# Performance work log

Measured on AMD Instinct MI355X. Metric: run time of the kernel, lower is better.

## Reference

```python
import jax, jax.numpy as jnp
import numpy as np

DIM = 1024
N_HEADS = 16
N_KV = 4
HEAD_DIM = 64
HIDDEN = 2048
N_EXP = 8
TOP_K = 2
B, T = 2, 1024
EPS = 1e-6


def rmsnorm(x, w):
    rms = jnp.sqrt(jnp.mean(x * x, axis=-1, keepdims=True) + EPS)
    return w * x / rms


def apply_rope(x, cos, sin):
    # x: [B, H, T, D]; cos/sin: [T, D//2]
    Tn = x.shape[2]
    c = cos[None, None, :Tn, :]
    s = sin[None, None, :Tn, :]
    xe = x[..., 0::2]
    xo = x[..., 1::2]
    re = xe * c - xo * s
    ro = xe * s + xo * c
    return jnp.stack([re, ro], axis=-1).reshape(x.shape)


def setup_inputs() -> dict:
    key = jax.random.key(0)
    ks = jax.random.split(key, 12)
    sd = DIM ** -0.5
    x = jax.random.normal(ks[0], (B, T, DIM), dtype=jnp.float32)
    # RoPE tables
    half = HEAD_DIM // 2
    inv_freq = 1.0 / (10000.0 ** (np.arange(0, half, dtype=np.float32) / half))
    pos = np.arange(T, dtype=np.float32)
    ang = np.outer(pos, inv_freq)
    cos = jnp.asarray(np.cos(ang), dtype=jnp.float32)
    sin = jnp.asarray(np.sin(ang), dtype=jnp.float32)
    return {
        "x": x,
        "cos": cos,
        "sin": sin,
        "norm_attn_w": jnp.ones((DIM,), jnp.float32),
        "wq": jax.random.normal(ks[1], (N_HEADS * HEAD_DIM, DIM), jnp.float32) * sd,
        "wk": jax.random.normal(ks[2], (N_KV * HEAD_DIM, DIM), jnp.float32) * sd,
        "wv": jax.random.normal(ks[3], (N_KV * HEAD_DIM, DIM), jnp.float32) * sd,
        "wo": jax.random.normal(ks[4], (DIM, N_HEADS * HEAD_DIM), jnp.float32) * sd,
        "norm_ffn_w": jnp.ones((DIM,), jnp.float32),
        "router_w": jax.random.normal(ks[5], (N_EXP, DIM), jnp.float32) * sd,
        "router_b": jnp.zeros((N_EXP,), jnp.float32),
        "w_gate": jax.random.normal(ks[6], (N_EXP, HIDDEN, DIM), jnp.float32) * sd,
        "w_up": jax.random.normal(ks[7], (N_EXP, HIDDEN, DIM), jnp.float32) * sd,
        "w_down": jax.random.normal(ks[8], (N_EXP, DIM, HIDDEN), jnp.float32) * (HIDDEN ** -0.5),
    }


def attention(x, cos, sin, wq, wk, wv, wo):
    Bn, Tn, _ = x.shape
    q = (x @ wq.T).reshape(Bn, Tn, N_HEADS, HEAD_DIM).transpose(0, 2, 1, 3)
    k = (x @ wk.T).reshape(Bn, Tn, N_KV, HEAD_DIM).transpose(0, 2, 1, 3)
    v = (x @ wv.T).reshape(Bn, Tn, N_KV, HEAD_DIM).transpose(0, 2, 1, 3)
    q = apply_rope(q, cos, sin)
    k = apply_rope(k, cos, sin)
    rep = N_HEADS // N_KV
    k = jnp.repeat(k, rep, axis=1)
    v = jnp.repeat(v, rep, axis=1)
    scale = HEAD_DIM ** -0.5
    scores = jnp.einsum("bhqd,bhkd->bhqk", q, k) * scale
    causal = jnp.triu(jnp.ones((Tn, Tn), dtype=bool), k=1)
    scores = jnp.where(causal[None, None], -jnp.inf, scores)
    attn = jax.nn.softmax(scores, axis=-1)
    out = jnp.einsum("bhqk,bhkd->bhqd", attn, v)
    out = out.transpose(0, 2, 1, 3).reshape(Bn, Tn, N_HEADS * HEAD_DIM)
    return out @ wo.T


def moe(x, router_w, router_b, w_gate, w_up, w_down):
    Bn, Tn, D = x.shape
    flat = x.reshape(-1, D)  # [N, D]
    N = flat.shape[0]
    logits = flat @ router_w.T + router_b
    probs = jax.nn.softmax(logits, axis=-1)
    top_vals, top_idx = jax.lax.top_k(probs, TOP_K)
    top_vals = top_vals / (jnp.sum(top_vals, axis=-1, keepdims=True) + 1e-9)
    # combine weights [N, E]
    comb = jnp.zeros((N, N_EXP), flat.dtype).at[jnp.arange(N)[:, None], top_idx].add(top_vals)
    g = jnp.einsum("nd,ehd->enh", flat, w_gate)
    u = jnp.einsum("nd,ehd->enh", flat, w_up)
    h = jax.nn.silu(g) * u
    eo = jnp.einsum("enh,edh->end", h, w_down)  # [E, N, D]
    out = jnp.einsum("ne,end->nd", comb, eo)
    return out.reshape(Bn, Tn, D)


def reference(x, cos, sin, norm_attn_w, wq, wk, wv, wo, norm_ffn_w, router_w, router_b, w_gate, w_up, w_down):
    x = x + attention(rmsnorm(x, norm_attn_w), cos, sin, wq, wk, wv, wo)
    x = x + moe(rmsnorm(x, norm_ffn_w), router_w, router_b, w_gate, w_up, w_down)
    return x
```

## Files before the change

### kernel.cpp

```cpp
#include <hip/hip_runtime.h>
#include <math.h>

#define N_TOK   2048
#define SEQ     1024
#define DIMM    1024
#define NH      16
#define NKV     4
#define HD      64
#define HID     2048
#define NEXP    8
#define QKVW    1536

typedef __attribute__((ext_vector_type(4))) float f32x4;
typedef __attribute__((ext_vector_type(8))) short s16x8;
typedef unsigned short u16;

__device__ __forceinline__ u16 f2bf(float f) {
    union { float f; unsigned u; } v; v.f = f;
    unsigned r = v.u + 0x7fffu + ((v.u >> 16) & 1u);
    return (u16)(r >> 16);
}
__device__ __forceinline__ float bf2f(u16 h) {
    union { unsigned u; float f; } v; v.u = ((unsigned)h) << 16;
    return v.f;
}

__device__ __forceinline__ f32x4 mfma16(s16x8 a, s16x8 b, f32x4 c) {
    return __builtin_amdgcn_mfma_f32_16x16x32_bf16(a, b, c, 0, 0, 0);
}

__device__ __forceinline__ int lds_byte(int row, int byte_in_row, int swz_key) {
    return row * 128 + (byte_in_row ^ ((swz_key & 7) << 4));
}

__device__ __forceinline__ s16x8 ldfrag(const char* base, int row, int ks, int lane) {
    int b = lds_byte(row, ks * 64 + ((lane >> 4) * 16), row);
    return *(const s16x8*)(base + b);
}

__device__ __forceinline__ void gload16(const void* g, void* l) {
    __builtin_amdgcn_global_load_lds(
        (const __attribute__((address_space(1))) void*)g,
        (__attribute__((address_space(3))) void*)l, 16, 0, 0);
}

__device__ __forceinline__ void cvt_chunk(int cb, int ncvt, int cvt_base, int cvt_end,
    const float* __restrict__ wg, const float* __restrict__ wu, const float* __restrict__ wd,
    u16* __restrict__ wgb, u16* __restrict__ wub, u16* __restrict__ wdb, int tid)
{
    const int n4 = 4 << 20;
    int i = cvt_base + cb * 1024 + tid;
    int stride = ncvt * 1024;
    for (; i < cvt_end; i += stride) {
        int seg = i >> 22;
        int j = i & (n4 - 1);
        const f32x4* in = (const f32x4*)((seg == 0) ? wg : (seg == 1) ? wu : wd);
        ushort4* out = (ushort4*)((seg == 0) ? wgb : (seg == 1) ? wub : wdb);
        f32x4 v0 = __builtin_nontemporal_load(in + j);
        f32x4 v1 = __builtin_nontemporal_load(in + j + 256);
        f32x4 v2 = __builtin_nontemporal_load(in + j + 512);
        f32x4 v3 = __builtin_nontemporal_load(in + j + 768);
        ushort4 o0, o1, o2, o3;
        o0.x = f2bf(v0[0]); o0.y = f2bf(v0[1]); o0.z = f2bf(v0[2]); o0.w = f2bf(v0[3]);
        o1.x = f2bf(v1[0]); o1.y = f2bf(v1[1]); o1.z = f2bf(v1[2]); o1.w = f2bf(v1[3]);
        o2.x = f2bf(v2[0]); o2.y = f2bf(v2[1]); o2.z = f2bf(v2[2]); o2.w = f2bf(v2[3]);
        o3.x = f2bf(v3[0]); o3.y = f2bf(v3[1]); o3.z = f2bf(v3[2]); o3.w = f2bf(v3[3]);
        out[j]       = o0;
        out[j + 256] = o1;
        out[j + 512] = o2;
        out[j + 768] = o3;
    }
}

__global__ __launch_bounds__(256) void prep1(const float* __restrict__ wq,
    const float* __restrict__ wk, const float* __restrict__ wv, const float* __restrict__ wo,
    u16* __restrict__ hi, u16* __restrict__ lo,
    const float* __restrict__ x, const float* __restrict__ w_na,
    u16* __restrict__ oh, u16* __restrict__ ol)
{
    if (blockIdx.x < 1024) {
        int i = blockIdx.x * 256 + threadIdx.x;
        int stride = 1024 * 256;
        for (; i < 655360; i += stride) {
            const float* in; int j;
            if (i < 262144)      { in = wq; j = i; }
            else if (i < 327680) { in = wk; j = i - 262144; }
            else if (i < 393216) { in = wv; j = i - 327680; }
            else                 { in = wo; j = i - 393216; }
            f32x4 v = __builtin_nontemporal_load((const f32x4*)in + j);
            ushort4 h, l;
            h.x = f2bf(v[0]); h.y = f2bf(v[1]); h.z = f2bf(v[2]); h.w = f2bf(v[3]);
            l.x = f2bf(v[0] - bf2f(h.x)); l.y = f2bf(v[1] - bf2f(h.y));
            l.z = f2bf(v[2] - bf2f(h.z)); l.w = f2bf(v[3] - bf2f(h.w));
            reinterpret_cast<ushort4*>(hi)[i] = h;
            reinterpret_cast<ushort4*>(lo)[i] = l;
        }
    } else {
        int row = blockIdx.x - 1024;
        const float4* xr = reinterpret_cast<const float4*>(x + (size_t)row * DIMM);
        const float4* wr = reinterpret_cast<const float4*>(w_na);
        float4 v = xr[threadIdx.x];
        float ss = v.x*v.x + v.y*v.y + v.z*v.z + v.w*v.w;
#pragma unroll
        for (int off = 32; off; off >>= 1) ss += __shfl_xor(ss, off);
        __shared__ float red[4];
        int wid = threadIdx.x >> 6, lane = threadIdx.x & 63;
        if (lane == 0) red[wid] = ss;
        __syncthreads();
        float tot = red[0] + red[1] + red[2] + red[3];
        float inv = rsqrtf(tot * (1.0f/DIMM) + 1e-6f);
        float4 ww = wr[threadIdx.x];
        float4 o;
        o.x = ww.x * v.x * inv;
        o.y = ww.y * v.y * inv;
        o.z = ww.z * v.z * inv;
        o.w = ww.w * v.w * inv;
        ushort4 h, l;
        h.x = f2bf(o.x); h.y = f2bf(o.y); h.z = f2bf(o.z); h.w = f2bf(o.w);
        l.x = f2bf(o.x - bf2f(h.x)); l.y = f2bf(o.y - bf2f(h.y));
        l.z = f2bf(o.z - bf2f(h.z)); l.w = f2bf(o.w - bf2f(h.w));
        reinterpret_cast<ushort4*>(oh + (size_t)row * DIMM)[threadIdx.x] = h;
        reinterpret_cast<ushort4*>(ol + (size_t)row * DIMM)[threadIdx.x] = l;
    }
}

__global__ __launch_bounds__(256) void rmsnorm_router(const float* __restrict__ x,
    const float* __restrict__ w, const float* __restrict__ rw, const float* __restrict__ rb,
    u16* __restrict__ outb, int* __restrict__ top_idx, float* __restrict__ top_w)
{
    int row = blockIdx.x;
    int tid = threadIdx.x;
    int wid = tid >> 6, lane = tid & 63;
    const float4* xr = reinterpret_cast<const float4*>(x + (size_t)row * DIMM);
    const float4* wr = reinterpret_cast<const float4*>(w);
    float4 v = xr[tid];
    float ss = v.x*v.x + v.y*v.y + v.z*v.z + v.w*v.w;
#pragma unroll
    for (int off = 32; off; off >>= 1) ss += __shfl_xor(ss, off);
    __shared__ float red[4];
    __shared__ float lred[4][NEXP];
    if (lane == 0) red[wid] = ss;
    __syncthreads();
    float tot = red[0] + red[1] + red[2] + red[3];
    float inv = rsqrtf(tot * (1.0f/DIMM) + 1e-6f);
    float4 ww = wr[tid];
    float4 o;
    o.x = ww.x * v.x * inv;
    o.y = ww.y * v.y * inv;
    o.z = ww.z * v.z * inv;
    o.w = ww.w * v.w * inv;
    ushort4 ob;
    ob.x = f2bf(o.x); ob.y = f2bf(o.y); ob.z = f2bf(o.z); ob.w = f2bf(o.w);
    reinterpret_cast<ushort4*>(outb + (size_t)row * DIMM)[tid] = ob;
    float acc[NEXP];
#pragma unroll
    for (int e = 0; e < NEXP; e++) {
        float4 r4 = reinterpret_cast<const float4*>(rw + (size_t)e * DIMM)[tid];
        acc[e] = o.x * r4.x + o.y * r4.y + o.z * r4.z + o.w * r4.w;
    }
#pragma unroll
    for (int e = 0; e < NEXP; e++) {
        float p = acc[e];
#pragma unroll
        for (int off = 32; off; off >>= 1) p += __shfl_xor(p, off);
        acc[e] = p;
    }
    if (lane == 0)
#pragma unroll
        for (int e = 0; e < NEXP; e++) lred[wid][e] = acc[e];
    __syncthreads();
    if (tid == 0) {
        float lg[NEXP];
#pragma unroll
        for (int e = 0; e < NEXP; e++)
            lg[e] = lred[0][e] + lred[1][e] + lred[2][e] + lred[3][e] + rb[e];
        float m = lg[0];
#pragma unroll
        for (int e = 1; e < NEXP; e++) m = fmaxf(m, lg[e]);
        float pe[NEXP], s = 0.f;
#pragma unroll
        for (int e = 0; e < NEXP; e++) { pe[e] = __expf(lg[e] - m); s += pe[e]; }
        int i1 = 0; float v1 = pe[0];
#pragma unroll
        for (int e = 1; e < NEXP; e++) if (pe[e] > v1) { v1 = pe[e]; i1 = e; }
        int i2 = -1; float v2 = -1.f;
#pragma unroll
        for (int e = 0; e < NEXP; e++) if (e != i1 && pe[e] > v2) { v2 = pe[e]; i2 = e; }
        v1 /= s; v2 /= s;
        float den = v1 + v2 + 1e-9f;
        top_idx[2 * row] = i1; top_idx[2 * row + 1] = i2;
        top_w[2 * row] = v1 / den; top_w[2 * row + 1] = v2 / den;
    }
}

__global__ __launch_bounds__(256) void route_build(const int* __restrict__ top_idx,
    const float* __restrict__ top_w, int* __restrict__ counts, int* __restrict__ offs,
    int* __restrict__ assign_token, float* __restrict__ assign_w)
{
    __shared__ int lcnt[NEXP], loff[NEXP], lpos[NEXP];
    int tid = threadIdx.x;
    if (tid < NEXP) { lcnt[tid] = 0; lpos[tid] = 0; }
    __syncthreads();
    for (int i = tid; i < 2 * N_TOK; i += 256)
        atomicAdd(&lcnt[top_idx[i]], 1);
    __syncthreads();
    if (tid == 0) {
        int s = 0;
        for (int e = 0; e < NEXP; e++) { loff[e] = s; s += lcnt[e]; }
    }
    __syncthreads();
    if (tid < NEXP) { counts[tid] = lcnt[tid]; offs[tid] = loff[tid]; }
    for (int i = tid; i < 2 * N_TOK; i += 256) {
        int e = top_idx[i];
        int p = atomicAdd(&lpos[e], 1);
        int r = loff[e] + p;
        assign_token[r] = i >> 1;
        assign_w[r] = top_w[i];
    }
}

__global__ __launch_bounds__(256) void gemm_cvt(const u16* __restrict__ Ah_,
    const u16* __restrict__ Al_, const u16* __restrict__ Bh_, const u16* __restrict__ Bl_,
    float* __restrict__ C, const float* __restrict__ R, int M, int N, int K, int ldc,
    int gx, int gy,
    const float* __restrict__ wg, const float* __restrict__ wu, const float* __restrict__ wd,
    u16* __restrict__ wgb, u16* __restrict__ wub, u16* __restrict__ wdb,
    int cvt_base, int cvt_end, int ncvt)
{
    int blk = blockIdx.x;
    if (blk >= gx * gy) {
        cvt_chunk(blk - gx * gy, ncvt, cvt_base, cvt_end, wg, wu, wd, wgb, wub, wdb, threadIdx.x);
        return;
    }
    __shared__ __align__(16) u16 Ah[128 * 64], Al[128 * 64];
    __shared__ __align__(16) u16 Bh[64 * 64],  Bl[64 * 64];
    int tid = threadIdx.x;
    int m0 = (blk / gx) * 128, n0 = (blk % gx) * 64;
    int lane = tid & 63, wv = tid >> 6;
    int wm = wv >> 1, wn = wv & 1;
    int sr = lane >> 3, sc = lane & 7;

    f32x4 acc[4][2];
#pragma unroll
    for (int i = 0; i < 4; i++)
#pragma unroll
        for (int j = 0; j < 2; j++) acc[i][j] = f32x4{0.f, 0.f, 0.f, 0.f};

    const int NT = K >> 6;
    int ph = (blk * 5) & (NT - 1);

    for (int tt = 0; tt < NT; ++tt) {
        int k0 = ((tt + ph) & (NT - 1)) << 6;
#pragma unroll
        for (int i = 0; i < 4; i++) {
            int row = wv * 32 + i * 8 + sr;
            int c = sc ^ (row & 7);
            size_t g = (size_t)(m0 + row) * K + k0 + c * 8;
            gload16(Ah_ + g, (void*)(Ah + (wv * 4 + i) * 512));
            gload16(Al_ + g, (void*)(Al + (wv * 4 + i) * 512));
        }
#pragma unroll
        for (int i = 0; i < 2; i++) {
            int row = wv * 16 + i * 8 + sr;
            int c = sc ^ (row & 7);
            size_t g = (size_t)(n0 + row) * K + k0 + c * 8;
            gload16(Bh_ + g, (void*)(Bh + (wv * 2 + i) * 512));
            gload16(Bl_ + g, (void*)(Bl + (wv * 2 + i) * 512));
        }
        __syncthreads();
#pragma unroll
        for (int ks = 0; ks < 2; ++ks) {
            s16x8 afh[4], afl[4], bfh[2], bfl[2];
#pragma unroll
            for (int mi = 0; mi < 4; mi++) {
                int row = wm * 64 + mi * 16 + (lane & 15);
                afh[mi] = ldfrag((const char*)Ah, row, ks, lane);
                afl[mi] = ldfrag((const char*)Al, row, ks, lane);
            }
#pragma unroll
            for (int nj = 0; nj < 2; nj++) {
                int row = wn * 32 + nj * 16 + (lane & 15);
                bfh[nj] = ldfrag((const char*)Bh, row, ks, lane);
                bfl[nj] = ldfrag((const char*)Bl, row, ks, lane);
            }
#pragma unroll
            for (int mi = 0; mi < 4; mi++)
#pragma unroll
                for (int nj = 0; nj < 2; nj++) {
                    acc[mi][nj] = mfma16(afl[mi], bfh[nj], acc[mi][nj]);
                    acc[mi][nj] = mfma16(afh[mi], bfl[nj], acc[mi][nj]);
                    acc[mi][nj] = mfma16(afh[mi], bfh[nj], acc[mi][nj]);
                }
        }
        __syncthreads();
    }
#pragma unroll
    for (int mi = 0; mi < 4; mi++)
#pragma unroll
        for (int nj = 0; nj < 2; nj++)
#pragma unroll
            for (int r = 0; r < 4; r++) {
                int m = m0 + wm * 64 + mi * 16 + (lane >> 4) * 4 + r;
                int n = n0 + wn * 32 + nj * 16 + (lane & 15);
                float v = acc[mi][nj][r];
                if (R) v += R[(size_t)m * ldc + n];
                C[(size_t)m * ldc + n] = v;
            }
}

__global__ __launch_bounds__(256) void prep2(const float* __restrict__ qkvb,
    const float* __restrict__ cs, const float* __restrict__ sn,
    u16* __restrict__ qsh, u16* __restrict__ qsl,
    u16* __restrict__ ksh, u16* __restrict__ ksl,
    u16* __restrict__ vth, u16* __restrict__ vtl)
{
    const int ROPE_BLOCKS = (N_TOK * (NH + NKV) * 32) / 256;
    if (blockIdx.x < ROPE_BLOCKS) {
        int gid = blockIdx.x * 256 + threadIdx.x;
        const int QTOT = N_TOK * NH * 32;
        int nheads, base_col, out_w;
        u16 *oh, *ol;
        if (gid < QTOT) {
            nheads = NH; base_col = 0; out_w = NH * HD; oh = qsh; ol = qsl;
        } else {
            gid -= QTOT;
            nheads = NKV; base_col = 1024; out_w = NKV * HD; oh = ksh; ol = ksl;
        }
        int i = gid & 31;
        int h = (gid >> 5) % nheads;
        int n = gid / (32 * nheads);
        int t = n & (SEQ - 1);
        const float* p = qkvb + (size_t)n * QKVW + base_col + h * HD + 2 * i;
        float xe = p[0], xo = p[1];
        float c = cs[t * 32 + i], s = sn[t * 32 + i];
        float re = xe * c - xo * s;
        float ro = xe * s + xo * c;
        size_t o = (size_t)n * out_w + h * HD + 2 * i;
        u16 reh = f2bf(re), roh = f2bf(ro);
        oh[o] = reh;     oh[o + 1] = roh;
        ol[o] = f2bf(re - bf2f(reh));
        ol[o + 1] = f2bf(ro - bf2f(roh));
    } else {
        __shared__ float t[64][65];
        int r = blockIdx.x - ROPE_BLOCKS;
        int bx = r & 31;
        int by = r >> 5;
        int tid = threadIdx.x;
        int c4 = tid & 15, r0 = tid >> 4;
#pragma unroll
        for (int i = 0; i < 4; i++) {
            int row = r0 + i * 16;
            float4 vv = *(const float4*)(qkvb + (size_t)(bx * 64 + row) * QKVW + 1280 + by * 64 + c4 * 4);
            t[c4 * 4 + 0][row] = vv.x;
            t[c4 * 4 + 1][row] = vv.y;
            t[c4 * 4 + 2][row] = vv.z;
            t[c4 * 4 + 3][row] = vv.w;
        }
        __syncthreads();
#pragma unroll
        for (int i = 0; i < 4; i++) {
            int drow = r0 + i * 16;
            ushort4 hh, ll;
            float a = t[drow][c4 * 4 + 0], b = t[drow][c4 * 4 + 1];
            float c = t[drow][c4 * 4 + 2], d = t[drow][c4 * 4 + 3];
            hh.x = f2bf(a); hh.y = f2bf(b); hh.z = f2bf(c); hh.w = f2bf(d);
            ll.x = f2bf(a - bf2f(hh.x)); ll.y = f2bf(b - bf2f(hh.y));
            ll.z = f2bf(c - bf2f(hh.z)); ll.w = f2bf(d - bf2f(hh.w));
            size_t o = ((size_t)(by * 64 + drow) * N_TOK + bx * 64 + c4 * 4) >> 2;
            reinterpret_cast<ushort4*>(vth)[o] = hh;
            reinterpret_cast<ushort4*>(vtl)[o] = ll;
        }
    }
}

__global__ __launch_bounds__(256) void attn_cvt(const u16* __restrict__ qsh,
    const u16* __restrict__ qsl, const u16* __restrict__ ksh, const u16* __restrict__ ksl,
    const u16* __restrict__ vth, const u16* __restrict__ vtl,
    u16* __restrict__ outh, u16* __restrict__ outl,
    const float* __restrict__ wg, const float* __restrict__ wu, const float* __restrict__ wd,
    u16* __restrict__ wgb, u16* __restrict__ wub, u16* __restrict__ wdb,
    int cvt_base, int cvt_end, int ncvt)
{
    if (blockIdx.x >= 512) {
        cvt_chunk(blockIdx.x - 512, ncvt, cvt_base, cvt_end, wg, wu, wd, wgb, wub, wdb, threadIdx.x);
        return;
    }
    int bi = blockIdx.x;
    int b = bi >> 8;
    int h = (bi >> 4) & 15;
    int qt = 15 - (bi & 15);
    int kvh = h >> 2;
    int tid = threadIdx.x;
    int lane = tid & 63, wv = tid >> 6;
    int q0 = qt * 64;
    int sr = lane >> 3, sc = lane & 7;

    __shared__ __align__(16) u16 Qh[64 * 64], Ql[64 * 64];
    __shared__ __align__(16) u16 Kh[64 * 64], Kl[64 * 64];
    __shared__ __align__(16) u16 Vh[64 * 64], Vl[64 * 64];

#pragma unroll
    for (int i = 0; i < 2; i++) {
        int row = wv * 16 + i * 8 + sr;
        int c = sc ^ (row & 7);
        size_t g = (size_t)(b * SEQ + q0 + row) * (NH * HD) + h * HD + c * 8;
        gload16(qsh + g, (void*)(Qh + (wv * 2 + i) * 512));
        gload16(qsl + g, (void*)(Ql + (wv * 2 + i) * 512));
    }
    __syncthreads();

    s16x8 aQh[2], aQl[2];
#pragma unroll
    for (int ks = 0; ks < 2; ks++) {
        aQh[ks] = ldfrag((const char*)Qh, wv * 16 + (lane & 15), ks, lane);
        aQl[ks] = ldfrag((const char*)Ql, wv * 16 + (lane & 15), ks, lane);
    }

    float m_run[4], l_run[4];
    f32x4 acc_o[4];
#pragma unroll
    for (int r = 0; r < 4; r++) { m_run[r] = -1e30f; l_run[r] = 0.f; }
#pragma unroll
    for (int nj = 0; nj < 4; nj++) acc_o[nj] = f32x4{0.f, 0.f, 0.f, 0.f};

    for (int kt = 0; kt <= qt; kt++) {
        int kbase = kt * 64;
        __syncthreads();
#pragma unroll
        for (int i = 0; i < 2; i++) {
            int row = wv * 16 + i * 8 + sr;
            int c = sc ^ (row & 7);
            size_t gk = (size_t)(b * SEQ + kbase + row) * (NKV * HD) + kvh * HD + c * 8;
            size_t gv = (size_t)(kvh * HD + row) * N_TOK + b * SEQ + kbase + c * 8;
            gload16(ksh + gk, (void*)(Kh + (wv * 2 + i) * 512));
            gload16(ksl + gk, (void*)(Kl + (wv * 2 + i) * 512));
            gload16(vth + gv, (void*)(Vh + (wv * 2 + i) * 512));
            gload16(vtl + gv, (void*)(Vl + (wv * 2 + i) * 512));
        }
        __syncthreads();

        f32x4 sacc[4];
#pragma unroll
        for (int nj = 0; nj < 4; nj++) sacc[nj] = f32x4{0.f, 0.f, 0.f, 0.f};
#pragma unroll
        for (int ks = 0; ks < 2; ks++) {
#pragma unroll
            for (int nj = 0; nj < 4; nj++) {
                s16x8 bKh = ldfrag((const char*)Kh, nj * 16 + (lane & 15), ks, lane);
                s16x8 bKl = ldfrag((const char*)Kl, nj * 16 + (lane & 15), ks, lane);
                sacc[nj] = mfma16(aQl[ks], bKh, sacc[nj]);
                sacc[nj] = mfma16(aQh[ks], bKl, sacc[nj]);
                sacc[nj] = mfma16(aQh[ks], bKh, sacc[nj]);
            }
        }

        float sv[4][4];
#pragma unroll
        for (int nj = 0; nj < 4; nj++)
#pragma unroll
            for (int r = 0; r < 4; r++) {
                float s = sacc[nj][r] * 0.125f;
                if (kt == qt) {
                    int row_loc = wv * 16 + (lane >> 4) * 4 + r;
                    int col_loc = nj * 16 + (lane & 15);
                    if (col_loc > row_loc) s = -1e30f;
                }
                sv[nj][r] = s;
            }

        float p[4][4];
#pragma unroll
        for (int r = 0; r < 4; r++) {
            float mx = fmaxf(fmaxf(sv[0][r], sv[1][r]), fmaxf(sv[2][r], sv[3][r]));
            mx = fmaxf(mx, __shfl_xor(mx, 1));
            mx = fmaxf(mx, __shfl_xor(mx, 2));
            mx = fmaxf(mx, __shfl_xor(mx, 4));
            mx = fmaxf(mx, __shfl_xor(mx, 8));
            float m_new = fmaxf(m_run[r], mx);
            float corr = __expf(m_run[r] - m_new);
            float ps = 0.f;
#pragma unroll
            for (int nj = 0; nj < 4; nj++) {
                float pv = __expf(sv[nj][r] - m_new);
                p[nj][r] = pv;
                ps += pv;
            }
            ps += __shfl_xor(ps, 1);
            ps += __shfl_xor(ps, 2);
            ps += __shfl_xor(ps, 4);
            ps += __shfl_xor(ps, 8);
            l_run[r] = l_run[r] * corr + ps;
            m_run[r] = m_new;
#pragma unroll
            for (int nj = 0; nj < 4; nj++) acc_o[nj][r] *= corr;
        }

        char* phb = (char*)Qh + wv * 2048;
        char* plb = (char*)Ql + wv * 2048;
#pragma unroll
        for (int nj = 0; nj < 4; nj++)
#pragma unroll
            for (int r = 0; r < 4; r++) {
                int row = (lane >> 4) * 4 + r;
                int col = nj * 16 + (lane & 15);
                u16 hh = f2bf(p[nj][r]);
                u16 ll = f2bf(p[nj][r] - bf2f(hh));
                int byte = lds_byte(row, col * 2, row);
                *(u16*)(phb + byte) = hh;
                *(u16*)(plb + byte) = ll;
            }

#pragma unroll
        for (int ks = 0; ks < 2; ks++) {
            s16x8 aPh = ldfrag(phb, lane & 15, ks, lane);
            s16x8 aPl = ldfrag(plb, lane & 15, ks, lane);
#pragma unroll
            for (int nj = 0; nj < 4; nj++) {
                s16x8 bVh = ldfrag((const char*)Vh, nj * 16 + (lane & 15), ks, lane);
                s16x8 bVl = ldfrag((const char*)Vl, nj * 16 + (lane & 15), ks, lane);
                acc_o[nj] = mfma16(aPl, bVh, acc_o[nj]);
                acc_o[nj] = mfma16(aPh, bVl, acc_o[nj]);
                acc_o[nj] = mfma16(aPh, bVh, acc_o[nj]);
            }
        }
    }

#pragma unroll
    for (int r = 0; r < 4; r++) {
        int row_glob = q0 + wv * 16 + (lane >> 4) * 4 + r;
        float inv = 1.f / l_run[r];
#pragma unroll
        for (int nj = 0; nj < 4; nj++) {
            int dv = nj * 16 + (lane & 15);
            size_t idx = (size_t)(b * SEQ + row_glob) * (NH * HD) + h * HD + dv;
            float v = acc_o[nj][r] * inv;
            u16 hh = f2bf(v);
            outh[idx] = hh;
            outl[idx] = f2bf(v - bf2f(hh));
        }
    }
}

__global__ __launch_bounds__(256, 4) void moe_gateup3(const u16* __restrict__ xb,
    const u16* __restrict__ wgb, const u16* __restrict__ wub,
    const int* __restrict__ assign_token, const int* __restrict__ offs,
    const int* __restrict__ counts, u16* __restrict__ hbufb)
{
    int e = blockIdx.z;
    int cnt = counts[e];
    int t0 = blockIdx.y * 64;
    if (t0 >= cnt) return;
    int base = offs[e];
    int h0 = blockIdx.x * 64;
    __shared__ __align__(16) u16 As[64 * 64];
    __shared__ __align__(16) u16 Gs[64 * 64];
    __shared__ __align__(16) u16 Us[64 * 64];
    __shared__ int toks[64];
    int tid = threadIdx.x;
    if (tid < 64) {
        int a = t0 + tid;
        toks[tid] = (a < cnt) ? assign_token[base + a] : 0;
    }
    __syncthreads();
    int lane = tid & 63, wv = tid >> 6;
    int wm = wv >> 1, wn = wv & 1;
    int sr = lane >> 3, sc = lane & 7;

    int tokr[2];
#pragma unroll
    for (int i = 0; i < 2; i++) tokr[i] = toks[wv * 16 + i * 8 + sr];

    const u16* wge = wgb + (size_t)e * HID * DIMM;
    const u16* wue = wub + (size_t)e * HID * DIMM;

    f32x4 accg[2][2], accu[2][2];
#pragma unroll
    for (int i = 0; i < 2; i++)
#pragma unroll
        for (int j = 0; j < 2; j++) { accg[i][j] = f32x4{0,0,0,0}; accu[i][j] = f32x4{0,0,0,0}; }

    const int NT = DIMM / 64;
    int bid = blockIdx.x + gridDim.x * (blockIdx.y + gridDim.y * blockIdx.z);
    int ph = (bid * 5) & (NT - 1);

    for (int tt = 0; tt < NT; ++tt) {
        int k0 = ((tt + ph) & (NT - 1)) << 6;
#pragma unroll
        for (int i = 0; i < 2; i++) {
            int row = wv * 16 + i * 8 + sr;
            int c = sc ^ (row & 7);
            gload16(xb + (size_t)tokr[i] * DIMM + k0 + c * 8, (void*)(As + (wv * 2 + i) * 512));
            gload16(wge + (size_t)(h0 + row) * DIMM + k0 + c * 8, (void*)(Gs + (wv * 2 + i) * 512));
            gload16(wue + (size_t)(h0 + row) * DIMM + k0 + c * 8, (void*)(Us + (wv * 2 + i) * 512));
        }
        __syncthreads();
#pragma unroll
        for (int ks = 0; ks < 2; ++ks) {
            s16x8 af[2], gf[2], uf[2];
#pragma unroll
            for (int mi = 0; mi < 2; mi++)
                af[mi] = ldfrag((const char*)As, wm * 32 + mi * 16 + (lane & 15), ks, lane);
#pragma unroll
            for (int nj = 0; nj < 2; nj++) {
                int row = wn * 32 + nj * 16 + (lane & 15);
                gf[nj] = ldfrag((const char*)Gs, row, ks, lane);
                uf[nj] = ldfrag((const char*)Us, row, ks, lane);
            }
#pragma unroll
            for (int mi = 0; mi < 2; mi++)
#pragma unroll
                for (int nj = 0; nj < 2; nj++) {
                    accg[mi][nj] = mfma16(af[mi], gf[nj], accg[mi][nj]);
                    accu[mi][nj] = mfma16(af[mi], uf[nj], accu[mi][nj]);
                }
        }
        __syncthreads();
    }
#pragma unroll
    for (int mi = 0; mi < 2; mi++)
#pragma unroll
        for (int nj = 0; nj < 2; nj++)
#pragma unroll
            for (int r = 0; r < 4; r++) {
                int row = wm * 32 + mi * 16 + (lane >> 4) * 4 + r;
                if (t0 + row < cnt) {
                    int col = wn * 32 + nj * 16 + (lane & 15);
                    float g = accg[mi][nj][r], u = accu[mi][nj][r];
                    float hh = (g / (1.f + __expf(-g))) * u;
                    hbufb[(size_t)(base + t0 + row) * HID + h0 + col] = f2bf(hh);
                }
            }
}

__global__ __launch_bounds__(256) void moe_down2(const u16* __restrict__ hbufb,
    const u16* __restrict__ wdb, const int* __restrict__ assign_token,
    const float* __restrict__ assign_w, const int* __restrict__ offs,
    const int* __restrict__ counts, float* __restrict__ out)
{
    int e = blockIdx.z;
    int cnt = counts[e];
    int t0 = blockIdx.y * 128;
    if (t0 >= cnt) return;
    int base = offs[e];
    int d0 = blockIdx.x * 128;
    __shared__ __align__(16) u16 As[128 * 64];
    __shared__ __align__(16) u16 Bs[128 * 64];
    __shared__ int toks[128];
    __shared__ float rw_[128];
    int tid = threadIdx.x;
    if (tid < 128) {
        int a = t0 + tid;
        toks[tid] = (a < cnt) ? assign_token[base + a] : 0;
        rw_[tid] = (a < cnt) ? assign_w[base + a] : 0.f;
    }
    __syncthreads();
    int lane = tid & 63, wv = tid >> 6;
    int wm = wv >> 1, wn = wv & 1;
    int sr = lane >> 3, sc = lane & 7;

    const u16* wde = wdb + (size_t)e * DIMM * HID;

    f32x4 acc[4][4];
#pragma unroll
    for (int i = 0; i < 4; i++)
#pragma unroll
        for (int j = 0; j < 4; j++) acc[i][j] = f32x4{0,0,0,0};

    const int NT = HID / 64;
    int bid = blockIdx.x + gridDim.x * (blockIdx.y + gridDim.y * blockIdx.z);
    int ph = (bid * 5) & (NT - 1);

    for (int tt = 0; tt < NT; ++tt) {
        int k0 = ((tt + ph) & (NT - 1)) << 6;
#pragma unroll
        for (int i = 0; i < 4; i++) {
            int row = wv * 32 + i * 8 + sr;
            int c = sc ^ (row & 7);
            gload16(hbufb + (size_t)(base + t0 + row) * HID + k0 + c * 8, (void*)(As + (wv * 4 + i) * 512));
            gload16(wde + (size_t)(d0 + row) * HID + k0 + c * 8, (void*)(Bs + (wv * 4 + i) * 512));
        }
        __syncthreads();
#pragma unroll
        for (int ks = 0; ks < 2; ++ks) {
            s16x8 af[4];
#pragma unroll
            for (int mi = 0; mi < 4; mi++)
                af[mi] = ldfrag((const char*)As, wm * 64 + mi * 16 + (lane & 15), ks, lane);
#pragma unroll
            for (int nj = 0; nj < 4; nj++) {
                s16x8 bf = ldfrag((const char*)Bs, wn * 64 + nj * 16 + (lane & 15), ks, lane);
#pragma unroll
                for (int mi = 0; mi < 4; mi++)
                    acc[mi][nj] = mfma16(af[mi], bf, acc[mi][nj]);
            }
        }
        __syncthreads();
    }
#pragma unroll
    for (int mi = 0; mi < 4; mi++)
#pragma unroll
        for (int r = 0; r < 4; r++) {
            int row = wm * 64 + mi * 16 + (lane >> 4) * 4 + r;
            if (t0 + row < cnt) {
                int tok = toks[row];
                float w = rw_[row];
#pragma unroll
                for (int nj = 0; nj < 4; nj++) {
                    int col = d0 + wn * 64 + nj * 16 + (lane & 15);
                    atomicAdd(&out[(size_t)tok * DIMM + col], acc[mi][nj][r] * w);
                }
            }
        }
}

extern "C" void kernel_launch(void* const* d_in, const int* in_sizes, int n_in,
                              void* d_out, int out_size, void* d_ws, size_t ws_size,
                              hipStream_t stream)
{
    const float* x      = (const float*)d_in[0];
    const float* cs     = (const float*)d_in[1];
    const float* sn     = (const float*)d_in[2];
    const float* w_na   = (const float*)d_in[3];
    const float* wq     = (const float*)d_in[4];
    const float* wk     = (const float*)d_in[5];
    const float* wv     = (const float*)d_in[6];
    const float* wo     = (const float*)d_in[7];
    const float* w_nf   = (const float*)d_in[8];
    const float* rw     = (const float*)d_in[9];
    const float* rb     = (const float*)d_in[10];
    const float* wg     = (const float*)d_in[11];
    const float* wu     = (const float*)d_in[12];
    const float* wd     = (const float*)d_in[13];
    float* out = (float*)d_out;

    const size_t F = 1024 * 1024;
    float* wsf = (float*)d_ws;

    float* qkvb = wsf;
    float* tail = wsf + 3 * F;
    u16* qsh    = (u16*)(wsf + 3 * F + F / 2);
    u16* qsl    = (u16*)(wsf + 4 * F + F / 2);
    u16* ksh    = (u16*)(wsf + 5 * F + F / 2);
    u16* ksl    = (u16*)(wsf + 5 * F + 3 * F / 4);
    u16* vth    = (u16*)(wsf + 6 * F);
    u16* vtl    = (u16*)(wsf + 6 * F + F / 4);
    u16* xn2b   = (u16*)(wsf + 6 * F + F / 2);
    u16* hbufb  = (u16*)(wsf + 7 * F + F / 2);
    u16* xnh    = (u16*)(wsf + 7 * F + F / 2);
    u16* xnl    = (u16*)(wsf + 8 * F + F / 2);
    u16* attnh  = (u16*)(wsf + 9 * F + F / 2);
    u16* attnl  = (u16*)(wsf + 10 * F + F / 2);
    u16* wgb    = (u16*)(wsf + 11 * F + F / 2);
    u16* wub    = (u16*)(wsf + 19 * F + F / 2);
    u16* wdb    = (u16*)(wsf + 27 * F + F / 2);
    u16* wqkvoh = (u16*)(wsf + 35 * F + F / 2);
    u16* wqkvol = (u16*)(wsf + 36 * F + 3 * F / 4);

    int*   top_idx      = (int*)tail;
    float* top_w        = tail + 4096;
    int*   counts       = (int*)(tail + 8192);
    int*   offs         = (int*)(tail + 8192) + 8;
    int*   assign_token = (int*)(tail + 8192) + 32;
    float* assign_w     = tail + 8192 + 32 + 4096;

    const int CV1 = 5767168;
    const int CV2 = 8912896;
    const int CV3 = 12582912;

    prep1<<<3072, 256, 0, stream>>>(wq, wk, wv, wo, wqkvoh, wqkvol, x, w_na, xnh, xnl);
    gemm_cvt<<<384 + 1280, 256, 0, stream>>>(xnh, xnl, wqkvoh, wqkvol,
                                             qkvb, nullptr, N_TOK, QKVW, DIMM, QKVW,
                                             QKVW / 64, 16,
                                             wg, wu, wd, wgb, wub, wdb, 0, CV1, 1280);
    prep2<<<5248, 256, 0, stream>>>(qkvb, cs, sn, qsh, qsl, ksh, ksl, vth, vtl);
    attn_cvt<<<1536, 256, 0, stream>>>(qsh, qsl, ksh, ksl, vth, vtl, attnh, attnl,
                                       wg, wu, wd, wgb, wub, wdb, CV1, CV2, 1024);
    gemm_cvt<<<256 + 768, 256, 0, stream>>>(attnh, attnl,
                                            wqkvoh + (size_t)1536 * 1024, wqkvol + (size_t)1536 * 1024,
                                            out, x, N_TOK, DIMM, NH * HD, DIMM,
                                            DIMM / 64, 16,
                                            wg, wu, wd, wgb, wub, wdb, CV2, CV3, 768);
    rmsnorm_router<<<N_TOK, 256, 0, stream>>>(out, w_nf, rw, rb, xn2b, top_idx, top_w);
    route_build<<<1, 256, 0, stream>>>(top_idx, top_w, counts, offs, assign_token, assign_w);
    moe_gateup3<<<dim3(HID / 64, 32, NEXP), 256, 0, stream>>>(xn2b, wgb, wub, assign_token, offs, counts, hbufb);
    moe_down2<<<dim3(DIMM / 128, 16, NEXP), 256, 0, stream>>>(hbufb, wdb, assign_token, assign_w, offs, counts, out);
}
```

Baseline: 292.8 us.

## Split long causal attention query tiles across two blocks with a combine pass

```diff
diff --git a/kernel.cpp b/kernel.cpp
--- a/kernel.cpp
+++ b/kernel.cpp
@@ -377,18 +377,32 @@
     const u16* __restrict__ qsl, const u16* __restrict__ ksh, const u16* __restrict__ ksl,
     const u16* __restrict__ vth, const u16* __restrict__ vtl,
     u16* __restrict__ outh, u16* __restrict__ outl,
+    float* __restrict__ pO, float* __restrict__ pM, float* __restrict__ pL,
     const float* __restrict__ wg, const float* __restrict__ wu, const float* __restrict__ wd,
     u16* __restrict__ wgb, u16* __restrict__ wub, u16* __restrict__ wdb,
     int cvt_base, int cvt_end, int ncvt)
 {
-    if (blockIdx.x >= 512) {
-        cvt_chunk(blockIdx.x - 512, ncvt, cvt_base, cvt_end, wg, wu, wd, wgb, wub, wdb, threadIdx.x);
+    if (blockIdx.x >= 768) {
+        cvt_chunk(blockIdx.x - 768, ncvt, cvt_base, cvt_end, wg, wu, wd, wgb, wub, wdb, threadIdx.x);
         return;
     }
     int bi = blockIdx.x;
-    int b = bi >> 8;
-    int h = (bi >> 4) & 15;
-    int qt = 15 - (bi & 15);
+    int b, h, qt, kt_lo, kt_hi;
+    bool partial;
+    if (bi < 512) {
+        int part = bi & 1;
+        int t = bi >> 1;
+        b = t >> 7; h = (t >> 3) & 15; qt = 15 - (t & 7);
+        int half = (qt + 1) >> 1;
+        kt_lo = part ? half : 0;
+        kt_hi = part ? qt : half - 1;
+        partial = true;
+    } else {
+        int idx = bi - 512;
+        b = idx >> 7; h = (idx >> 3) & 15; qt = 7 - (idx & 7);
+        kt_lo = 0; kt_hi = qt;
+        partial = false;
+    }
     int kvh = h >> 2;
     int tid = threadIdx.x;
     int lane = tid & 63, wv = tid >> 6;
@@ -423,7 +437,7 @@
 #pragma unroll
     for (int nj = 0; nj < 4; nj++) acc_o[nj] = f32x4{0.f, 0.f, 0.f, 0.f};
 
-    for (int kt = 0; kt <= qt; kt++) {
+    for (int kt = kt_lo; kt <= kt_hi; kt++) {
         int kbase = kt * 64;
         __syncthreads();
 #pragma unroll
@@ -525,19 +539,63 @@
         }
     }
 
-#pragma unroll
-    for (int r = 0; r < 4; r++) {
-        int row_glob = q0 + wv * 16 + (lane >> 4) * 4 + r;
-        float inv = 1.f / l_run[r];
-#pragma unroll
-        for (int nj = 0; nj < 4; nj++) {
-            int dv = nj * 16 + (lane & 15);
-            size_t idx = (size_t)(b * SEQ + row_glob) * (NH * HD) + h * HD + dv;
-            float v = acc_o[nj][r] * inv;
-            u16 hh = f2bf(v);
-            outh[idx] = hh;
-            outl[idx] = f2bf(v - bf2f(hh));
-        }
+    if (partial) {
+        float* pOt = pO + (size_t)bi * 4096;
+#pragma unroll
+        for (int r = 0; r < 4; r++) {
+            int row = wv * 16 + (lane >> 4) * 4 + r;
+#pragma unroll
+            for (int nj = 0; nj < 4; nj++) {
+                int col = nj * 16 + (lane & 15);
+                pOt[row * 64 + col] = acc_o[nj][r];
+            }
+            if ((lane & 15) == 0) {
+                pM[bi * 64 + row] = m_run[r];
+                pL[bi * 64 + row] = l_run[r];
+            }
+        }
+    } else {
+#pragma unroll
+        for (int r = 0; r < 4; r++) {
+            int row_glob = q0 + wv * 16 + (lane >> 4) * 4 + r;
+            float inv = 1.f / l_run[r];
+#pragma unroll
+            for (int nj = 0; nj < 4; nj++) {
+                int dv = nj * 16 + (lane & 15);
+                size_t idx = (size_t)(b * SEQ + row_glob) * (NH * HD) + h * HD + dv;
+                float v = acc_o[nj][r] * inv;
+                u16 hh = f2bf(v);
+                outh[idx] = hh;
+                outl[idx] = f2bf(v - bf2f(hh));
+            }
+        }
+    }
+}
+
+__global__ __launch_bounds__(256) void attn_combine(const float* __restrict__ pO,
+    const float* __restrict__ pM, const float* __restrict__ pL,
+    u16* __restrict__ outh, u16* __restrict__ outl)
+{
+    int t = blockIdx.x;
+    int b = t >> 7, h = (t >> 3) & 15, qt = 15 - (t & 7);
+    int q0 = qt * 64;
+    int tid = threadIdx.x;
+    int row = tid >> 2, cg = (tid & 3) * 16;
+    int s0 = 2 * t, s1 = 2 * t + 1;
+    float m0 = pM[s0 * 64 + row], l0 = pL[s0 * 64 + row];
+    float m1 = pM[s1 * 64 + row], l1 = pL[s1 * 64 + row];
+    float m = fmaxf(m0, m1);
+    float c0 = __expf(m0 - m), c1 = __expf(m1 - m);
+    float inv = 1.f / (l0 * c0 + l1 * c1);
+    const float* O0 = pO + ((size_t)s0 * 64 + row) * 64 + cg;
+    const float* O1 = pO + ((size_t)s1 * 64 + row) * 64 + cg;
+    size_t ob = (size_t)(b * SEQ + q0 + row) * (NH * HD) + h * HD + cg;
+#pragma unroll
+    for (int j = 0; j < 16; j++) {
+        float v = (O0[j] * c0 + O1[j] * c1) * inv;
+        u16 hh = f2bf(v);
+        outh[ob + j] = hh;
+        outl[ob + j] = f2bf(v - bf2f(hh));
     }
 }
 
@@ -763,6 +821,10 @@
     int*   assign_token = (int*)(tail + 8192) + 32;
     float* assign_w     = tail + 8192 + 32 + 4096;
 
+    float* pO = qkvb;
+    float* pM = qkvb + 2097152;
+    float* pL = qkvb + 2097152 + 32768;
+
     const int CV1 = 5767168;
     const int CV2 = 8912896;
     const int CV3 = 12582912;
@@ -773,8 +835,10 @@
                                              QKVW / 64, 16,
                                              wg, wu, wd, wgb, wub, wdb, 0, CV1, 1280);
     prep2<<<5248, 256, 0, stream>>>(qkvb, cs, sn, qsh, qsl, ksh, ksl, vth, vtl);
-    attn_cvt<<<1536, 256, 0, stream>>>(qsh, qsl, ksh, ksl, vth, vtl, attnh, attnl,
+    attn_cvt<<<1792, 256, 0, stream>>>(qsh, qsl, ksh, ksl, vth, vtl, attnh, attnl,
+                                       pO, pM, pL,
                                        wg, wu, wd, wgb, wub, wdb, CV1, CV2, 1024);
+    attn_combine<<<256, 256, 0, stream>>>(pO, pM, pL, attnh, attnl);
     gemm_cvt<<<256 + 768, 256, 0, stream>>>(attnh, attnl,
                                             wqkvoh + (size_t)1536 * 1024, wqkvol + (size_t)1536 * 1024,
                                             out, x, N_TOK, DIMM, NH * HD, DIMM,
```

New measurement: 283.1 us. -3.3%, faster.
